# Kernel optimization log

Measured on AMD Instinct MI355X. Metric: run time of the kernel, lower is better.

The kernel has to match this reference:

```python
import jax, jax.numpy as jnp
import numpy as np

E = 200000   # edges (trade events)
N = 20000    # nodes
H = 128      # hidden_dim / memory_dim / time_dim
EF = 32      # edge_feat_dim
T = 14       # price_seq_dim
P = 4        # num_parties
S = 50       # num_states
LH = 32      # LSTM hidden


def setup_inputs() -> dict:
    key = jax.random.key(0)
    ks = jax.random.split(key, 32)
    rn = lambda k, shape, s=0.02: jax.random.normal(k, shape, dtype=jnp.float32) * s
    return {
        'src': jax.random.randint(ks[0], (E,), 0, N),
        'dst': jax.random.randint(ks[1], (E,), 0, N),
        't': jax.random.uniform(ks[2], (E,), dtype=jnp.float32) * 100.0,
        'msg': jax.random.normal(ks[3], (E, EF), dtype=jnp.float32),
        'price_seq': jax.random.normal(ks[4], (E, T), dtype=jnp.float32),
        'trade_t': jax.random.uniform(ks[5], (E,), dtype=jnp.float32),
        'x_static': jax.random.randint(ks[6], (N, 2), 0, P),
        # TGN memory state
        'memory': rn(ks[7], (N, H), 0.05),
        'last_update': jnp.zeros((N,), jnp.float32),
        # time encoder (cos(w*dt + b)), time_dim = H
        'time_w': rn(ks[8], (H,), 1.0),
        'time_b': rn(ks[9], (H,), 1.0),
        # GRU memory updater: input = [mem_src, mem_dst, raw_msg, t_enc] -> 3H+EF
        'gru_Wih': rn(ks[10], (3 * H, 3 * H + EF)),
        'gru_Whh': rn(ks[11], (3 * H, H)),
        'gru_bih': rn(ks[12], (3 * H,)),
        'gru_bhh': rn(ks[13], (3 * H,)),
        # static features
        'party_emb': rn(ks[14], (P, 16), 0.1),
        'state_emb': rn(ks[15], (S, 16), 0.1),
        'static_W': rn(ks[16], (H, 32)),
        'static_b': rn(ks[17], (H,)),
        # price LSTM (input_size=1, hidden=32); torch gate order i,f,g,o
        'lstm_Wih': rn(ks[18], (4 * LH, 1), 0.1),
        'lstm_Whh': rn(ks[19], (4 * LH, LH), 0.1),
        'lstm_bih': rn(ks[20], (4 * LH,), 0.1),
        'lstm_bhh': rn(ks[21], (4 * LH,), 0.1),
        'price_W': rn(ks[22], (H, LH)),
        'price_b': rn(ks[23], (H,)),
        # predictor MLP (dropout inactive at inference)
        'pred_W1': rn(ks[24], (64, 3 * H)),
        'pred_b1': rn(ks[25], (64,)),
        'pred_W2': rn(ks[26], (1, 64)),
        'pred_b2': rn(ks[27], (1,)),
    }


def reference(src, dst, t, msg, price_seq, trade_t, x_static,
              memory, last_update, time_w, time_b,
              gru_Wih, gru_Whh, gru_bih, gru_bhh,
              party_emb, state_emb, static_W, static_b,
              lstm_Wih, lstm_Whh, lstm_bih, lstm_bhh,
              price_W, price_b, pred_W1, pred_b1, pred_W2, pred_b2):
    n_nodes = memory.shape[0]

    # --- TGN memory update: scatter per-edge messages, GRU update, gather ---
    t_enc = lambda dt: jnp.cos(dt[:, None] * time_w[None, :] + time_b)  # [E,H]
    m_src, m_dst = memory[src], memory[dst]
    msg_to_dst = jnp.concatenate([m_src, m_dst, msg, t_enc(t - last_update[dst])], axis=1)
    msg_to_src = jnp.concatenate([m_dst, m_src, msg, t_enc(t - last_update[src])], axis=1)
    idx = jnp.concatenate([dst, src])                       # [2E]
    all_msgs = jnp.concatenate([msg_to_dst, msg_to_src], 0)  # [2E, 3H+EF]
    summed = jax.ops.segment_sum(all_msgs, idx, num_segments=n_nodes)
    count = jax.ops.segment_sum(jnp.ones((idx.shape[0],), jnp.float32), idx, num_segments=n_nodes)
    agg = summed / jnp.maximum(count, 1.0)[:, None]          # mean-aggregated message per node

    # GRUCell(agg, memory), torch semantics
    gi = agg @ gru_Wih.T + gru_bih
    gh = memory @ gru_Whh.T + gru_bhh
    i_r, i_z, i_n = jnp.split(gi, 3, axis=1)
    h_r, h_z, h_n = jnp.split(gh, 3, axis=1)
    r = jax.nn.sigmoid(i_r + h_r)
    z = jax.nn.sigmoid(i_z + h_z)
    n = jnp.tanh(i_n + r * h_n)
    h_new = (1.0 - z) * n + z * memory
    mem_new = jnp.where((count > 0)[:, None], h_new, memory)

    mem_src = mem_new[src]
    mem_dst = mem_new[dst]

    # --- static branch ---
    static_feat = jnp.concatenate([party_emb[x_static[src, 0]], state_emb[x_static[src, 1]]], axis=1)
    src_static = static_feat @ static_W.T + static_b

    # --- price LSTM branch ---
    e, lh = price_seq.shape[0], lstm_Whh.shape[1]

    def step(carry, x_t):
        h, c = carry
        g = x_t @ lstm_Wih.T + lstm_bih + h @ lstm_Whh.T + lstm_bhh
        gi_, gf_, gg_, go_ = jnp.split(g, 4, axis=1)
        c = jax.nn.sigmoid(gf_) * c + jax.nn.sigmoid(gi_) * jnp.tanh(gg_)
        h = jax.nn.sigmoid(go_) * jnp.tanh(c)
        return (h, c), None

    xs = price_seq.T[:, :, None]  # [T, E, 1]
    z0 = jnp.zeros((e, lh), price_seq.dtype)
    (h_n_last, _), _ = jax.lax.scan(step, (z0, z0), xs)
    price_emb = h_n_last @ price_W.T + price_b

    # --- fusion + predictor ---
    pol_ctx = mem_src + src_static
    comp_ctx = mem_dst + price_emb
    combined = jnp.concatenate([pol_ctx, comp_ctx, price_emb], axis=1)
    hid = jax.nn.relu(combined @ pred_W1.T + pred_b1)
    out = hid @ pred_W2.T + pred_b2
    return out.squeeze(-1)
```

## Files before the change

kernel.cpp:

```cpp
#include <hip/hip_runtime.h>

#define H 128
#define EF 32
#define TT 14
#define LH 32
#define KDIM 416
#define GOUT 512
#define KTOT 544
#define KP 288

typedef __attribute__((ext_vector_type(8))) short bf16x8;
typedef __attribute__((ext_vector_type(4))) float f32x4;

__device__ __forceinline__ float sigmoidf_(float x) {
  float e = __builtin_amdgcn_exp2f(x * -1.442695041f);
  return __builtin_amdgcn_rcpf(1.0f + e);
}
__device__ __forceinline__ float tanhfast_(float x) {
  float e = __builtin_amdgcn_exp2f(x * 2.885390082f);
  return 1.0f - 2.0f * __builtin_amdgcn_rcpf(e + 1.0f);
}
__device__ __forceinline__ ushort f2bf(float x) {
  uint u = __float_as_uint(x);
  u += 0x7fff + ((u >> 16) & 1);
  return (ushort)(u >> 16);
}

__global__ __launch_bounds__(256) void build_weights(
    const float* __restrict__ Wih, const float* __restrict__ Whh,
    ushort* __restrict__ WcatT) {
  int i = blockIdx.x * 256 + threadIdx.x;
  if (i >= GOUT * KTOT) return;
  int o = i / KTOT, k = i % KTOT;
  int j = o & 127;
  float v = 0.f;
  if (o < 256) {
    int row = (o < 128) ? j : (128 + j);
    v = (k < KDIM) ? Wih[row * KDIM + k] : Whh[row * H + (k - KDIM)];
  } else if (o < 384) {
    v = (k < KDIM) ? Wih[(256 + j) * KDIM + k] : 0.f;
  } else {
    v = (k < KDIM) ? 0.f : Whh[(256 + j) * H + (k - KDIM)];
  }
  WcatT[i] = f2bf(v);
}

__global__ __launch_bounds__(256) void prep_pred(
    const float* __restrict__ W1, const float* __restrict__ b1,
    const float* __restrict__ static_W, const float* __restrict__ static_b,
    const float* __restrict__ price_W, const float* __restrict__ price_b,
    const float* __restrict__ party_emb, const float* __restrict__ state_emb,
    ushort* __restrict__ Wcombb, float* __restrict__ tab_p, float* __restrict__ tab_s,
    float* __restrict__ bias2) {
  __shared__ float G1[64][32];
  int tid = threadIdx.x;
  for (int idx = tid; idx < 2048; idx += 256) {
    int o = idx >> 5, k = idx & 31;
    float g = 0.f, m = 0.f;
    for (int j = 0; j < 128; j++) {
      g = fmaf(W1[o * 384 + j], static_W[j * 32 + k], g);
      m = fmaf(W1[o * 384 + 128 + j] + W1[o * 384 + 256 + j], price_W[j * 32 + k], m);
    }
    G1[o][k] = g;
    Wcombb[o * KP + 256 + k] = f2bf(m);
  }
  for (int idx = tid; idx < 64 * 256; idx += 256) {
    int o = idx >> 8, j = idx & 255;
    Wcombb[o * KP + j] = f2bf(W1[o * 384 + j]);
  }
  __syncthreads();
  for (int idx = tid; idx < 4 * 64; idx += 256) {
    int p = idx >> 6, o = idx & 63;
    float s = 0.f;
    for (int k = 0; k < 16; k++) s = fmaf(G1[o][k], party_emb[p * 16 + k], s);
    tab_p[idx] = s;
  }
  for (int idx = tid; idx < 50 * 64; idx += 256) {
    int si = idx >> 6, o = idx & 63;
    float s = 0.f;
    for (int k = 0; k < 16; k++) s = fmaf(G1[o][16 + k], state_emb[si * 16 + k], s);
    tab_s[idx] = s;
  }
  if (tid < 64) {
    float s = b1[tid];
    for (int j = 0; j < 128; j++) {
      s = fmaf(W1[tid * 384 + j], static_b[j], s);
      s = fmaf(W1[tid * 384 + 128 + j] + W1[tid * 384 + 256 + j], price_b[j], s);
    }
    bias2[tid] = s;
  }
}

__global__ void count_kernel(const int* __restrict__ src, const int* __restrict__ dst,
                             int* cnt, int E) {
  int e = blockIdx.x * blockDim.x + threadIdx.x;
  if (e < E) {
    atomicAdd(&cnt[dst[e]], 1);
    atomicAdd(&cnt[src[e]], 1);
  }
}

__global__ __launch_bounds__(1024) void scan_kernel(const int* __restrict__ cnt,
                                                    int* __restrict__ offs,
                                                    int* __restrict__ cursor, int N) {
  __shared__ int part[1024];
  int tid = threadIdx.x;
  int chunk = (N + 1023) / 1024;
  int beg = tid * chunk;
  int end = min(beg + chunk, N);
  int s = 0;
  for (int i = beg; i < end; i++) s += cnt[i];
  part[tid] = s;
  __syncthreads();
  for (int d = 1; d < 1024; d <<= 1) {
    int v = (tid >= d) ? part[tid - d] : 0;
    __syncthreads();
    part[tid] += v;
    __syncthreads();
  }
  int run = (tid > 0) ? part[tid - 1] : 0;
  for (int i = beg; i < end; i++) {
    offs[i] = run;
    cursor[i] = run;
    run += cnt[i];
  }
  if (tid == 1023) offs[N] = part[1023];
}

__global__ void fill_kernel(const int* __restrict__ src, const int* __restrict__ dst,
                            int* cursor, int* __restrict__ other, int* __restrict__ eid, int E) {
  int e = blockIdx.x * blockDim.x + threadIdx.x;
  if (e >= E) return;
  int s = src[e], d = dst[e];
  int p1 = atomicAdd(&cursor[d], 1);
  other[p1] = s; eid[p1] = e;
  int p2 = atomicAdd(&cursor[s], 1);
  other[p2] = d; eid[p2] = e;
}

__global__ __launch_bounds__(512) void agg_kernel(
    const int* __restrict__ offs, const int* __restrict__ other, const int* __restrict__ eid,
    const float* __restrict__ mem, const float* __restrict__ msg,
    const float* __restrict__ t, const float* __restrict__ lu,
    const float* __restrict__ tw, const float* __restrict__ tb,
    const int* __restrict__ cnt, ushort* __restrict__ agg_b, int N) {
  __shared__ int ld_oth[256];
  __shared__ int ld_eid[256];
  __shared__ float red[16 * 292];
  int tid = threadIdx.x;
  int grp = tid >> 5;
  int l = tid & 31;
  int v = blockIdx.x;
  int beg = offs[v], end = offs[v + 1];
  int deg = end - beg;
  int ndeg = min(deg, 256);
  for (int i = tid; i < ndeg; i += 512) {
    ld_oth[i] = other[beg + i];
    ld_eid[i] = eid[beg + i];
  }
  __syncthreads();

  float lupd = lu[v];
  float4 w4 = *reinterpret_cast<const float4*>(tw + 4 * l);
  float4 b4 = *reinterpret_cast<const float4*>(tb + 4 * l);
  float a0q0 = 0.f, a0q1 = 0.f, a0q2 = 0.f, a0q3 = 0.f;
  float ac0 = 0.f, ac1 = 0.f, ac2 = 0.f, ac3 = 0.f;
  float amsg = 0.f;
  for (int p = grp; p < deg; p += 16) {
    int u, e;
    if (p < 256) { u = ld_oth[p]; e = ld_eid[p]; }
    else { u = other[beg + p]; e = eid[beg + p]; }
    float4 mrow = *reinterpret_cast<const float4*>(mem + (size_t)u * H + 4 * l);
    float te = t[e];
    amsg += msg[e * EF + l];
    float dt = te - lupd;
    a0q0 += mrow.x; a0q1 += mrow.y; a0q2 += mrow.z; a0q3 += mrow.w;
    ac0 += __cosf(fmaf(dt, w4.x, b4.x));
    ac1 += __cosf(fmaf(dt, w4.y, b4.y));
    ac2 += __cosf(fmaf(dt, w4.z, b4.z));
    ac3 += __cosf(fmaf(dt, w4.w, b4.w));
  }
  float* r = red + grp * 292;
  r[4 * l + 0] = a0q0; r[4 * l + 1] = a0q1; r[4 * l + 2] = a0q2; r[4 * l + 3] = a0q3;
  r[128 + 4 * l + 0] = ac0; r[128 + 4 * l + 1] = ac1;
  r[128 + 4 * l + 2] = ac2; r[128 + 4 * l + 3] = ac3;
  r[256 + l] = amsg;
  __syncthreads();

  int cv = cnt[v];
  float inv = 1.f / (float)max(cv, 1);
  ushort* arow = agg_b + (size_t)v * KTOT;
  if (tid < 288) {
    float s = 0.f;
#pragma unroll
    for (int g2 = 0; g2 < 16; g2++) s += red[g2 * 292 + tid];
    s *= inv;
    if (tid < 128) arow[tid] = f2bf(s);
    else if (tid < 256) arow[288 + (tid - 128)] = f2bf(s);
    else arow[256 + (tid - 256)] = f2bf(s);
  } else if (tid < 416) {
    int c = tid - 288;
    float mv = mem[(size_t)v * H + c];
    arow[128 + c] = f2bf((cv > 0) ? mv : 0.f);
    arow[416 + c] = f2bf(mv);
  }
}

__global__ __launch_bounds__(256) void gru_gemm_mfma(
    const ushort* __restrict__ aggb, const ushort* __restrict__ WcatT,
    const float* __restrict__ mem, const int* __restrict__ cnt,
    const float* __restrict__ bih, const float* __restrict__ bhh,
    ushort* __restrict__ mem_newb, int N) {
  __shared__ union {
    ushort a[32 * 552];
    float g[4][32][132];
  } sm;
  int tid = threadIdx.x;
  int lane = tid & 63;
  int w = tid >> 6;
  int n0 = blockIdx.x * 32;

#pragma unroll
  for (int i = 0; i < 8; i++) {
    int row = w * 8 + i;
    int gr = min(n0 + row, N - 1);
    const uint4* srcp = reinterpret_cast<const uint4*>(aggb + (size_t)gr * KTOT);
    uint4* dstp = reinterpret_cast<uint4*>(sm.a + row * 552);
    dstp[lane] = srcp[lane];
    if (lane < 4) dstp[64 + lane] = srcp[64 + lane];
  }
  __syncthreads();

  f32x4 acc[2][8] = {};
  int arow_b = (lane & 15);
  int koff = (lane >> 4) * 8;
  for (int ks = 0; ks < 17; ks++) {
    int k = ks * 32 + koff;
    bf16x8 afr0 = *reinterpret_cast<const bf16x8*>(sm.a + (arow_b) * 552 + k);
    bf16x8 afr1 = *reinterpret_cast<const bf16x8*>(sm.a + (16 + arow_b) * 552 + k);
#pragma unroll
    for (int nt = 0; nt < 8; nt++) {
      int o = w * 128 + nt * 16 + (lane & 15);
      bf16x8 bfr = *reinterpret_cast<const bf16x8*>(WcatT + (size_t)o * KTOT + k);
      acc[0][nt] = __builtin_amdgcn_mfma_f32_16x16x32_bf16(afr0, bfr, acc[0][nt], 0, 0, 0);
      acc[1][nt] = __builtin_amdgcn_mfma_f32_16x16x32_bf16(afr1, bfr, acc[1][nt], 0, 0, 0);
    }
  }
  __syncthreads();

#pragma unroll
  for (int mt = 0; mt < 2; mt++)
#pragma unroll
    for (int nt = 0; nt < 8; nt++)
#pragma unroll
      for (int r = 0; r < 4; r++)
        sm.g[w][mt * 16 + (lane >> 4) * 4 + r][nt * 16 + (lane & 15)] = acc[mt][nt][r];
  __syncthreads();

  int row = tid >> 3, j0 = (tid & 7) * 16;
  int n = n0 + row;
  if (n < N) {
    int cv = cnt[n];
#pragma unroll
    for (int jj = 0; jj < 16; jj++) {
      int j = j0 + jj;
      float m = mem[(size_t)n * H + j];
      float o;
      if (cv > 0) {
        float rp = sm.g[0][row][j] + bih[j] + bhh[j];
        float zp = sm.g[1][row][j] + bih[128 + j] + bhh[128 + j];
        float ip = sm.g[2][row][j] + bih[256 + j];
        float hp = sm.g[3][row][j] + bhh[256 + j];
        float r = sigmoidf_(rp), z = sigmoidf_(zp);
        float nn = tanhfast_(ip + r * hp);
        o = (1.f - z) * nn + z * m;
      } else {
        o = m;
      }
      mem_newb[(size_t)n * H + j] = f2bf(o);
    }
  }
}

__global__ __launch_bounds__(256) void lstm_mfma_kernel(
    const float* __restrict__ price_seq,
    const float* __restrict__ lWih, const float* __restrict__ lWhh,
    const float* __restrict__ lbih, const float* __restrict__ lbhh,
    ushort* __restrict__ houtb, int E) {
  __shared__ float ps[64][15];
  int tid = threadIdx.x;
  int lane = tid & 63;
  int el = lane & 15;
  int g = lane >> 4;
  int wv = tid >> 6;
  int row0 = blockIdx.x * 64;
  int el_local = wv * 16 + el;
  int e = row0 + el_local;
  bool valid = (e < E);

  for (int idx = tid; idx < 64 * TT; idx += 256) {
    int row = idx / TT, col = idx % TT;
    int ee = min(row0 + row, E - 1);
    ps[row][col] = price_seq[(size_t)ee * TT + col];
  }
  __syncthreads();

  union { uint u[4]; bf16x8 v; } afr[8];
#pragma unroll
  for (int b = 0; b < 8; b++) {
    const float* wr = lWhh + (16 * b + el) * LH + g * 8;
#pragma unroll
    for (int q = 0; q < 4; q++) {
      float lo = wr[2 * q], hi = wr[2 * q + 1];
      asm("v_cvt_pk_bf16_f32 %0, %1, %2" : "=v"(afr[b].u[q]) : "v"(lo), "v"(hi));
    }
  }
  uint afr2w[8];
#pragma unroll
  for (int b = 0; b < 8; b++) {
    float wvv = lWih[16 * b + el];
    float bv = lbih[16 * b + el] + lbhh[16 * b + el];
    uint pk;
    asm("v_cvt_pk_bf16_f32 %0, %1, %2" : "=v"(pk) : "v"(wvv), "v"(bv));
    afr2w[b] = (g == 0) ? pk : 0u;
  }

  int addr_i[4];
#pragma unroll
  for (int i = 0; i < 4; i++) addr_i[i] = (el + 16 * ((g & 1) * 2 + (i >> 1))) << 2;
  bool hi_sel = (g >> 1) != 0;

  float cst[8];
#pragma unroll
  for (int i = 0; i < 8; i++) cst[i] = 0.f;
  uint hpk[4] = {0u, 0u, 0u, 0u};
  const f32x4 zero4 = {0.f, 0.f, 0.f, 0.f};

#pragma unroll 1
  for (int t = 0; t < TT; t++) {
    union { uint u[4]; bf16x8 v; } bfr;
#pragma unroll
    for (int i = 0; i < 4; i++) {
      uint lo = (uint)__builtin_amdgcn_ds_bpermute(addr_i[i], (int)hpk[i & 1]);
      uint hi = (uint)__builtin_amdgcn_ds_bpermute(addr_i[i], (int)hpk[2 + (i & 1)]);
      bfr.u[i] = hi_sel ? hi : lo;
    }
    float x = ps[el_local][t];
    union { uint u[4]; bf16x8 v; } bfr2;
    uint xp;
    asm("v_cvt_pk_bf16_f32 %0, %1, %2" : "=v"(xp) : "v"(x), "v"(1.0f));
    bfr2.u[0] = (g == 0) ? xp : 0u;
    bfr2.u[1] = 0u; bfr2.u[2] = 0u; bfr2.u[3] = 0u;

    float hval[8];
    f32x4 acc0, acc1, acc2, acc3, acc4, acc5, acc6, acc7;
#define STEPACC(b, A) \
    { union { uint u[4]; bf16x8 v; } a2; a2.u[0] = afr2w[b]; a2.u[1] = 0u; a2.u[2] = 0u; a2.u[3] = 0u; \
      A = __builtin_amdgcn_mfma_f32_16x16x32_bf16(a2.v, bfr2.v, zero4, 0, 0, 0); \
      A = __builtin_amdgcn_mfma_f32_16x16x32_bf16(afr[b].v, bfr.v, A, 0, 0, 0); }
    STEPACC(0, acc0) STEPACC(1, acc1) STEPACC(2, acc2) STEPACC(3, acc3)
    STEPACC(4, acc4) STEPACC(5, acc5) STEPACC(6, acc6) STEPACC(7, acc7)
#undef STEPACC
#define NONLIN(b1, AI, AF, AG, AO) \
    { _Pragma("unroll") for (int r = 0; r < 4; r++) { \
        int mi = 4 * b1 + r; \
        float ig = sigmoidf_(AI[r]); \
        float fg = sigmoidf_(AF[r]); \
        float gg = tanhfast_(AG[r]); \
        float og = sigmoidf_(AO[r]); \
        float cv = fmaf(fg, cst[mi], ig * gg); \
        cst[mi] = cv; \
        hval[mi] = og * tanhfast_(cv); } }
    NONLIN(0, acc0, acc2, acc4, acc6)
    NONLIN(1, acc1, acc3, acc5, acc7)
#undef NONLIN
#pragma unroll
    for (int i = 0; i < 4; i++)
      asm("v_cvt_pk_bf16_f32 %0, %1, %2" : "=v"(hpk[i]) : "v"(hval[2 * i]), "v"(hval[2 * i + 1]));
  }

  if (valid) {
    uint2* rowp = reinterpret_cast<uint2*>(houtb + (size_t)e * LH);
    rowp[g] = make_uint2(hpk[0], hpk[1]);
    rowp[4 + g] = make_uint2(hpk[2], hpk[3]);
  }
}

__global__ __launch_bounds__(256) void pred_mfma(
    const int* __restrict__ src, const int* __restrict__ dst,
    const int* __restrict__ x_static,
    const ushort* __restrict__ mem_newb, const ushort* __restrict__ houtb,
    const ushort* __restrict__ Wcombb, const float* __restrict__ tab_p,
    const float* __restrict__ tab_s, const float* __restrict__ bias2,
    const float* __restrict__ W2, const float* __restrict__ b2,
    float* __restrict__ out, int E) {
  __shared__ ushort Asm[64 * 296];
  __shared__ int pidx[64], stix[64];
  __shared__ int sidx[64], didx[64];
  int tid = threadIdx.x;
  int row0 = blockIdx.x * 64;
  if (tid < 64) {
    int e = min(row0 + tid, E - 1);
    int s = src[e], d = dst[e];
    sidx[tid] = s; didx[tid] = d;
    pidx[tid] = x_static[s * 2]; stix[tid] = x_static[s * 2 + 1];
  }
  __syncthreads();
#pragma unroll
  for (int i = 0; i < 9; i++) {
    int idx = tid + i * 256;
    int row = idx / 36, c = idx % 36;
    int e = min(row0 + row, E - 1);
    uint4 v;
    if (c < 16) v = reinterpret_cast<const uint4*>(mem_newb + (size_t)sidx[row] * H)[c];
    else if (c < 32) v = reinterpret_cast<const uint4*>(mem_newb + (size_t)didx[row] * H)[c - 16];
    else v = reinterpret_cast<const uint4*>(houtb + (size_t)e * LH)[c - 32];
    *reinterpret_cast<uint4*>(Asm + row * 296 + c * 8) = v;
  }
  __syncthreads();

  int lane = tid & 63;
  int w = tid >> 6;
  f32x4 acc[4] = {};
  int arow = w * 16 + (lane & 15);
  int koff = (lane >> 4) * 8;
  for (int ks = 0; ks < 9; ks++) {
    int k = ks * 32 + koff;
    bf16x8 afr = *reinterpret_cast<const bf16x8*>(Asm + arow * 296 + k);
#pragma unroll
    for (int nt = 0; nt < 4; nt++) {
      int o = nt * 16 + (lane & 15);
      bf16x8 bfr = *reinterpret_cast<const bf16x8*>(Wcombb + (size_t)o * KP + k);
      acc[nt] = __builtin_amdgcn_mfma_f32_16x16x32_bf16(afr, bfr, acc[nt], 0, 0, 0);
    }
  }
  int ocol = lane & 15;
  float bb2 = b2[0];
#pragma unroll
  for (int r = 0; r < 4; r++) {
    int rl = w * 16 + (lane >> 4) * 4 + r;
    int p = pidx[rl], st = stix[rl];
    float s = 0.f;
#pragma unroll
    for (int nt = 0; nt < 4; nt++) {
      int o = nt * 16 + ocol;
      float hv = acc[nt][r] + bias2[o] + tab_p[p * 64 + o] + tab_s[st * 64 + o];
      s = fmaf(fmaxf(hv, 0.f), W2[o], s);
    }
#pragma unroll
    for (int d = 1; d < 16; d <<= 1) s += __shfl_xor(s, d);
    int e = row0 + rl;
    if (ocol == 0 && e < E) out[e] = s + bb2;
  }
}

extern "C" void kernel_launch(void* const* d_in, const int* in_sizes, int n_in,
                              void* d_out, int out_size, void* d_ws, size_t ws_size,
                              hipStream_t stream) {
  const int* src = (const int*)d_in[0];
  const int* dst = (const int*)d_in[1];
  const float* t = (const float*)d_in[2];
  const float* msg = (const float*)d_in[3];
  const float* price_seq = (const float*)d_in[4];
  const int* x_static = (const int*)d_in[6];
  const float* memory = (const float*)d_in[7];
  const float* last_update = (const float*)d_in[8];
  const float* time_w = (const float*)d_in[9];
  const float* time_b = (const float*)d_in[10];
  const float* gWih = (const float*)d_in[11];
  const float* gWhh = (const float*)d_in[12];
  const float* gbih = (const float*)d_in[13];
  const float* gbhh = (const float*)d_in[14];
  const float* party_emb = (const float*)d_in[15];
  const float* state_emb = (const float*)d_in[16];
  const float* static_W = (const float*)d_in[17];
  const float* static_b = (const float*)d_in[18];
  const float* lWih = (const float*)d_in[19];
  const float* lWhh = (const float*)d_in[20];
  const float* lbih = (const float*)d_in[21];
  const float* lbhh = (const float*)d_in[22];
  const float* price_W = (const float*)d_in[23];
  const float* price_b = (const float*)d_in[24];
  const float* W1 = (const float*)d_in[25];
  const float* b1 = (const float*)d_in[26];
  const float* W2 = (const float*)d_in[27];
  const float* b2 = (const float*)d_in[28];
  float* out = (float*)d_out;

  const int E = in_sizes[0];
  const int N = in_sizes[8];

  char* ws = (char*)d_ws;
  size_t off = 0;
  auto alloc = [&](size_t bytes) { size_t o = off; off += (bytes + 255) & ~(size_t)255; return o; };
  int* cnt       = (int*)(ws + alloc((size_t)N * 4));
  int* offs      = (int*)(ws + alloc((size_t)(N + 1) * 4));
  int* cursor    = (int*)(ws + alloc((size_t)N * 4));
  int* other     = (int*)(ws + alloc((size_t)2 * E * 4));
  int* eid       = (int*)(ws + alloc((size_t)2 * E * 4));
  ushort* WcatT  = (ushort*)(ws + alloc((size_t)GOUT * KTOT * 2));
  ushort* Wcombb = (ushort*)(ws + alloc((size_t)64 * KP * 2));
  float* tab_p   = (float*)(ws + alloc((size_t)4 * 64 * 4));
  float* tab_s   = (float*)(ws + alloc((size_t)50 * 64 * 4));
  float* bias2   = (float*)(ws + alloc((size_t)64 * 4));
  ushort* agg_b  = (ushort*)(ws + alloc((size_t)N * KTOT * 2));
  ushort* mem_newb = (ushort*)(ws + alloc((size_t)N * H * 2));
  ushort* houtb  = (ushort*)(ws + alloc((size_t)E * LH * 2));
  (void)ws_size;

  hipMemsetAsync(cnt, 0, (size_t)N * 4, stream);

  build_weights<<<(GOUT * KTOT + 255) / 256, 256, 0, stream>>>(gWih, gWhh, WcatT);
  prep_pred<<<1, 256, 0, stream>>>(W1, b1, static_W, static_b, price_W, price_b,
                                   party_emb, state_emb, Wcombb, tab_p, tab_s, bias2);
  count_kernel<<<(E + 255) / 256, 256, 0, stream>>>(src, dst, cnt, E);
  scan_kernel<<<1, 1024, 0, stream>>>(cnt, offs, cursor, N);
  fill_kernel<<<(E + 255) / 256, 256, 0, stream>>>(src, dst, cursor, other, eid, E);
  agg_kernel<<<N, 512, 0, stream>>>(offs, other, eid, memory, msg, t, last_update,
                                    time_w, time_b, cnt, agg_b, N);
  gru_gemm_mfma<<<(N + 31) / 32, 256, 0, stream>>>(agg_b, WcatT, memory, cnt,
                                                   gbih, gbhh, mem_newb, N);
  lstm_mfma_kernel<<<(E + 63) / 64, 256, 0, stream>>>(price_seq, lWih, lWhh, lbih, lbhh, houtb, E);
  pred_mfma<<<(E + 63) / 64, 256, 0, stream>>>(src, dst, x_static, mem_newb, houtb,
      Wcombb, tab_p, tab_s, bias2, W2, b2, out, E);
}
```

Measured before the change: 445.9 us.

## Fuse LSTM into aggregation launch and parallelize prep_pred across blocks

```diff
diff --git a/kernel.cpp b/kernel.cpp
--- a/kernel.cpp
+++ b/kernel.cpp
@@ -52,42 +52,48 @@
     const float* __restrict__ party_emb, const float* __restrict__ state_emb,
     ushort* __restrict__ Wcombb, float* __restrict__ tab_p, float* __restrict__ tab_s,
     float* __restrict__ bias2) {
-  __shared__ float G1[64][32];
+  __shared__ float G1s[4][32];
   int tid = threadIdx.x;
-  for (int idx = tid; idx < 2048; idx += 256) {
-    int o = idx >> 5, k = idx & 31;
+  int ob = blockIdx.x * 4;
+  if (tid < 128) {
+    int ol = tid >> 5, k = tid & 31;
+    int o = ob + ol;
     float g = 0.f, m = 0.f;
     for (int j = 0; j < 128; j++) {
       g = fmaf(W1[o * 384 + j], static_W[j * 32 + k], g);
       m = fmaf(W1[o * 384 + 128 + j] + W1[o * 384 + 256 + j], price_W[j * 32 + k], m);
     }
-    G1[o][k] = g;
+    G1s[ol][k] = g;
     Wcombb[o * KP + 256 + k] = f2bf(m);
   }
-  for (int idx = tid; idx < 64 * 256; idx += 256) {
-    int o = idx >> 8, j = idx & 255;
+  for (int idx = tid; idx < 1024; idx += 256) {
+    int ol = idx >> 8, j = idx & 255;
+    int o = ob + ol;
     Wcombb[o * KP + j] = f2bf(W1[o * 384 + j]);
   }
   __syncthreads();
-  for (int idx = tid; idx < 4 * 64; idx += 256) {
-    int p = idx >> 6, o = idx & 63;
-    float s = 0.f;
-    for (int k = 0; k < 16; k++) s = fmaf(G1[o][k], party_emb[p * 16 + k], s);
-    tab_p[idx] = s;
-  }
-  for (int idx = tid; idx < 50 * 64; idx += 256) {
-    int si = idx >> 6, o = idx & 63;
-    float s = 0.f;
-    for (int k = 0; k < 16; k++) s = fmaf(G1[o][16 + k], state_emb[si * 16 + k], s);
-    tab_s[idx] = s;
-  }
-  if (tid < 64) {
-    float s = b1[tid];
+  for (int idx = tid; idx < 216; idx += 256) {
+    if (idx < 16) {
+      int p = idx >> 2, ol = idx & 3;
+      float s = 0.f;
+      for (int k = 0; k < 16; k++) s = fmaf(G1s[ol][k], party_emb[p * 16 + k], s);
+      tab_p[p * 64 + ob + ol] = s;
+    } else {
+      int i2 = idx - 16;
+      int si = i2 >> 2, ol = i2 & 3;
+      float s = 0.f;
+      for (int k = 0; k < 16; k++) s = fmaf(G1s[ol][16 + k], state_emb[si * 16 + k], s);
+      tab_s[si * 64 + ob + ol] = s;
+    }
+  }
+  if (tid < 4) {
+    int o = ob + tid;
+    float s = b1[o];
     for (int j = 0; j < 128; j++) {
-      s = fmaf(W1[tid * 384 + j], static_b[j], s);
-      s = fmaf(W1[tid * 384 + 128 + j] + W1[tid * 384 + 256 + j], price_b[j], s);
-    }
-    bias2[tid] = s;
+      s = fmaf(W1[o * 384 + j], static_b[j], s);
+      s = fmaf(W1[o * 384 + 128 + j] + W1[o * 384 + 256 + j], price_b[j], s);
+    }
+    bias2[o] = s;
   }
 }
 
@@ -138,71 +144,175 @@
   other[p2] = d; eid[p2] = e;
 }
 
-__global__ __launch_bounds__(512) void agg_kernel(
+__global__ __launch_bounds__(512) void agg_lstm_kernel(
     const int* __restrict__ offs, const int* __restrict__ other, const int* __restrict__ eid,
     const float* __restrict__ mem, const float* __restrict__ msg,
     const float* __restrict__ t, const float* __restrict__ lu,
     const float* __restrict__ tw, const float* __restrict__ tb,
-    const int* __restrict__ cnt, ushort* __restrict__ agg_b, int N) {
-  __shared__ int ld_oth[256];
-  __shared__ int ld_eid[256];
-  __shared__ float red[16 * 292];
+    const int* __restrict__ cnt, ushort* __restrict__ agg_b, int N,
+    const float* __restrict__ price_seq,
+    const float* __restrict__ lWih, const float* __restrict__ lWhh,
+    const float* __restrict__ lbih, const float* __restrict__ lbhh,
+    ushort* __restrict__ houtb, int E, int nL) {
+  __shared__ union {
+    struct { int ld_oth[256]; int ld_eid[256]; float red[16 * 292]; } a;
+    float ps[128][15];
+  } sm;
   int tid = threadIdx.x;
-  int grp = tid >> 5;
-  int l = tid & 31;
-  int v = blockIdx.x;
-  int beg = offs[v], end = offs[v + 1];
-  int deg = end - beg;
-  int ndeg = min(deg, 256);
-  for (int i = tid; i < ndeg; i += 512) {
-    ld_oth[i] = other[beg + i];
-    ld_eid[i] = eid[beg + i];
-  }
-  __syncthreads();
-
-  float lupd = lu[v];
-  float4 w4 = *reinterpret_cast<const float4*>(tw + 4 * l);
-  float4 b4 = *reinterpret_cast<const float4*>(tb + 4 * l);
-  float a0q0 = 0.f, a0q1 = 0.f, a0q2 = 0.f, a0q3 = 0.f;
-  float ac0 = 0.f, ac1 = 0.f, ac2 = 0.f, ac3 = 0.f;
-  float amsg = 0.f;
-  for (int p = grp; p < deg; p += 16) {
-    int u, e;
-    if (p < 256) { u = ld_oth[p]; e = ld_eid[p]; }
-    else { u = other[beg + p]; e = eid[beg + p]; }
-    float4 mrow = *reinterpret_cast<const float4*>(mem + (size_t)u * H + 4 * l);
-    float te = t[e];
-    amsg += msg[e * EF + l];
-    float dt = te - lupd;
-    a0q0 += mrow.x; a0q1 += mrow.y; a0q2 += mrow.z; a0q3 += mrow.w;
-    ac0 += __cosf(fmaf(dt, w4.x, b4.x));
-    ac1 += __cosf(fmaf(dt, w4.y, b4.y));
-    ac2 += __cosf(fmaf(dt, w4.z, b4.z));
-    ac3 += __cosf(fmaf(dt, w4.w, b4.w));
-  }
-  float* r = red + grp * 292;
-  r[4 * l + 0] = a0q0; r[4 * l + 1] = a0q1; r[4 * l + 2] = a0q2; r[4 * l + 3] = a0q3;
-  r[128 + 4 * l + 0] = ac0; r[128 + 4 * l + 1] = ac1;
-  r[128 + 4 * l + 2] = ac2; r[128 + 4 * l + 3] = ac3;
-  r[256 + l] = amsg;
-  __syncthreads();
-
-  int cv = cnt[v];
-  float inv = 1.f / (float)max(cv, 1);
-  ushort* arow = agg_b + (size_t)v * KTOT;
-  if (tid < 288) {
-    float s = 0.f;
-#pragma unroll
-    for (int g2 = 0; g2 < 16; g2++) s += red[g2 * 292 + tid];
-    s *= inv;
-    if (tid < 128) arow[tid] = f2bf(s);
-    else if (tid < 256) arow[288 + (tid - 128)] = f2bf(s);
-    else arow[256 + (tid - 256)] = f2bf(s);
-  } else if (tid < 416) {
-    int c = tid - 288;
-    float mv = mem[(size_t)v * H + c];
-    arow[128 + c] = f2bf((cv > 0) ? mv : 0.f);
-    arow[416 + c] = f2bf(mv);
+
+  if ((int)blockIdx.x < nL) {
+    int lane = tid & 63;
+    int el = lane & 15;
+    int g = lane >> 4;
+    int wv = tid >> 6;
+    int row0 = blockIdx.x * 128;
+    int el_local = wv * 16 + el;
+    int e = row0 + el_local;
+    bool valid = (e < E);
+
+    for (int idx = tid; idx < 128 * TT; idx += 512) {
+      int row = idx / TT, col = idx % TT;
+      int ee = min(row0 + row, E - 1);
+      sm.ps[row][col] = price_seq[(size_t)ee * TT + col];
+    }
+    __syncthreads();
+
+    union { uint u[4]; bf16x8 v; } afr[8];
+#pragma unroll
+    for (int b = 0; b < 8; b++) {
+      const float* wr = lWhh + (16 * b + el) * LH + g * 8;
+#pragma unroll
+      for (int q = 0; q < 4; q++) {
+        float lo = wr[2 * q], hi = wr[2 * q + 1];
+        asm("v_cvt_pk_bf16_f32 %0, %1, %2" : "=v"(afr[b].u[q]) : "v"(lo), "v"(hi));
+      }
+    }
+    uint afr2w[8];
+#pragma unroll
+    for (int b = 0; b < 8; b++) {
+      float wvv = lWih[16 * b + el];
+      float bv = lbih[16 * b + el] + lbhh[16 * b + el];
+      uint pk;
+      asm("v_cvt_pk_bf16_f32 %0, %1, %2" : "=v"(pk) : "v"(wvv), "v"(bv));
+      afr2w[b] = (g == 0) ? pk : 0u;
+    }
+
+    int addr_i[4];
+#pragma unroll
+    for (int i = 0; i < 4; i++) addr_i[i] = (el + 16 * ((g & 1) * 2 + (i >> 1))) << 2;
+    bool hi_sel = (g >> 1) != 0;
+
+    float cst[8];
+#pragma unroll
+    for (int i = 0; i < 8; i++) cst[i] = 0.f;
+    uint hpk[4] = {0u, 0u, 0u, 0u};
+    const f32x4 zero4 = {0.f, 0.f, 0.f, 0.f};
+
+#pragma unroll 1
+    for (int tt = 0; tt < TT; tt++) {
+      union { uint u[4]; bf16x8 v; } bfr;
+#pragma unroll
+      for (int i = 0; i < 4; i++) {
+        uint lo = (uint)__builtin_amdgcn_ds_bpermute(addr_i[i], (int)hpk[i & 1]);
+        uint hi = (uint)__builtin_amdgcn_ds_bpermute(addr_i[i], (int)hpk[2 + (i & 1)]);
+        bfr.u[i] = hi_sel ? hi : lo;
+      }
+      float x = sm.ps[el_local][tt];
+      union { uint u[4]; bf16x8 v; } bfr2;
+      uint xp;
+      asm("v_cvt_pk_bf16_f32 %0, %1, %2" : "=v"(xp) : "v"(x), "v"(1.0f));
+      bfr2.u[0] = (g == 0) ? xp : 0u;
+      bfr2.u[1] = 0u; bfr2.u[2] = 0u; bfr2.u[3] = 0u;
+
+      float hval[8];
+      f32x4 acc0, acc1, acc2, acc3, acc4, acc5, acc6, acc7;
+#define STEPACC(b, A) \
+      { union { uint u[4]; bf16x8 v; } a2; a2.u[0] = afr2w[b]; a2.u[1] = 0u; a2.u[2] = 0u; a2.u[3] = 0u; \
+        A = __builtin_amdgcn_mfma_f32_16x16x32_bf16(a2.v, bfr2.v, zero4, 0, 0, 0); \
+        A = __builtin_amdgcn_mfma_f32_16x16x32_bf16(afr[b].v, bfr.v, A, 0, 0, 0); }
+      STEPACC(0, acc0) STEPACC(1, acc1) STEPACC(2, acc2) STEPACC(3, acc3)
+      STEPACC(4, acc4) STEPACC(5, acc5) STEPACC(6, acc6) STEPACC(7, acc7)
+#undef STEPACC
+#define NONLIN(b1, AI, AF, AG, AO) \
+      { _Pragma("unroll") for (int r = 0; r < 4; r++) { \
+          int mi = 4 * b1 + r; \
+          float ig = sigmoidf_(AI[r]); \
+          float fg = sigmoidf_(AF[r]); \
+          float gg = tanhfast_(AG[r]); \
+          float og = sigmoidf_(AO[r]); \
+          float cv = fmaf(fg, cst[mi], ig * gg); \
+          cst[mi] = cv; \
+          hval[mi] = og * tanhfast_(cv); } }
+      NONLIN(0, acc0, acc2, acc4, acc6)
+      NONLIN(1, acc1, acc3, acc5, acc7)
+#undef NONLIN
+#pragma unroll
+      for (int i = 0; i < 4; i++)
+        asm("v_cvt_pk_bf16_f32 %0, %1, %2" : "=v"(hpk[i]) : "v"(hval[2 * i]), "v"(hval[2 * i + 1]));
+    }
+
+    if (valid) {
+      uint2* rowp = reinterpret_cast<uint2*>(houtb + (size_t)e * LH);
+      rowp[g] = make_uint2(hpk[0], hpk[1]);
+      rowp[4 + g] = make_uint2(hpk[2], hpk[3]);
+    }
+  } else {
+    int grp = tid >> 5;
+    int l = tid & 31;
+    int v = blockIdx.x - nL;
+    int beg = offs[v], end = offs[v + 1];
+    int deg = end - beg;
+    int ndeg = min(deg, 256);
+    for (int i = tid; i < ndeg; i += 512) {
+      sm.a.ld_oth[i] = other[beg + i];
+      sm.a.ld_eid[i] = eid[beg + i];
+    }
+    __syncthreads();
+
+    float lupd = lu[v];
+    float4 w4 = *reinterpret_cast<const float4*>(tw + 4 * l);
+    float4 b4 = *reinterpret_cast<const float4*>(tb + 4 * l);
+    float a0q0 = 0.f, a0q1 = 0.f, a0q2 = 0.f, a0q3 = 0.f;
+    float ac0 = 0.f, ac1 = 0.f, ac2 = 0.f, ac3 = 0.f;
+    float amsg = 0.f;
+    for (int p = grp; p < deg; p += 16) {
+      int u, e;
+      if (p < 256) { u = sm.a.ld_oth[p]; e = sm.a.ld_eid[p]; }
+      else { u = other[beg + p]; e = eid[beg + p]; }
+      float4 mrow = *reinterpret_cast<const float4*>(mem + (size_t)u * H + 4 * l);
+      float te = t[e];
+      amsg += msg[e * EF + l];
+      float dt = te - lupd;
+      a0q0 += mrow.x; a0q1 += mrow.y; a0q2 += mrow.z; a0q3 += mrow.w;
+      ac0 += __cosf(fmaf(dt, w4.x, b4.x));
+      ac1 += __cosf(fmaf(dt, w4.y, b4.y));
+      ac2 += __cosf(fmaf(dt, w4.z, b4.z));
+      ac3 += __cosf(fmaf(dt, w4.w, b4.w));
+    }
+    float* r = sm.a.red + grp * 292;
+    r[4 * l + 0] = a0q0; r[4 * l + 1] = a0q1; r[4 * l + 2] = a0q2; r[4 * l + 3] = a0q3;
+    r[128 + 4 * l + 0] = ac0; r[128 + 4 * l + 1] = ac1;
+    r[128 + 4 * l + 2] = ac2; r[128 + 4 * l + 3] = ac3;
+    r[256 + l] = amsg;
+    __syncthreads();
+
+    int cv = cnt[v];
+    float inv = 1.f / (float)max(cv, 1);
+    ushort* arow = agg_b + (size_t)v * KTOT;
+    if (tid < 288) {
+      float s = 0.f;
+#pragma unroll
+      for (int g2 = 0; g2 < 16; g2++) s += sm.a.red[g2 * 292 + tid];
+      s *= inv;
+      if (tid < 128) arow[tid] = f2bf(s);
+      else if (tid < 256) arow[288 + (tid - 128)] = f2bf(s);
+      else arow[256 + (tid - 256)] = f2bf(s);
+    } else if (tid < 416) {
+      int c = tid - 288;
+      float mv = mem[(size_t)v * H + c];
+      arow[128 + c] = f2bf((cv > 0) ? mv : 0.f);
+      arow[416 + c] = f2bf(mv);
+    }
   }
 }
 
@@ -279,110 +389,6 @@
       }
       mem_newb[(size_t)n * H + j] = f2bf(o);
     }
-  }
-}
-
-__global__ __launch_bounds__(256) void lstm_mfma_kernel(
-    const float* __restrict__ price_seq,
-    const float* __restrict__ lWih, const float* __restrict__ lWhh,
-    const float* __restrict__ lbih, const float* __restrict__ lbhh,
-    ushort* __restrict__ houtb, int E) {
-  __shared__ float ps[64][15];
-  int tid = threadIdx.x;
-  int lane = tid & 63;
-  int el = lane & 15;
-  int g = lane >> 4;
-  int wv = tid >> 6;
-  int row0 = blockIdx.x * 64;
-  int el_local = wv * 16 + el;
-  int e = row0 + el_local;
-  bool valid = (e < E);
-
-  for (int idx = tid; idx < 64 * TT; idx += 256) {
-    int row = idx / TT, col = idx % TT;
-    int ee = min(row0 + row, E - 1);
-    ps[row][col] = price_seq[(size_t)ee * TT + col];
-  }
-  __syncthreads();
-
-  union { uint u[4]; bf16x8 v; } afr[8];
-#pragma unroll
-  for (int b = 0; b < 8; b++) {
-    const float* wr = lWhh + (16 * b + el) * LH + g * 8;
-#pragma unroll
-    for (int q = 0; q < 4; q++) {
-      float lo = wr[2 * q], hi = wr[2 * q + 1];
-      asm("v_cvt_pk_bf16_f32 %0, %1, %2" : "=v"(afr[b].u[q]) : "v"(lo), "v"(hi));
-    }
-  }
-  uint afr2w[8];
-#pragma unroll
-  for (int b = 0; b < 8; b++) {
-    float wvv = lWih[16 * b + el];
-    float bv = lbih[16 * b + el] + lbhh[16 * b + el];
-    uint pk;
-    asm("v_cvt_pk_bf16_f32 %0, %1, %2" : "=v"(pk) : "v"(wvv), "v"(bv));
-    afr2w[b] = (g == 0) ? pk : 0u;
-  }
-
-  int addr_i[4];
-#pragma unroll
-  for (int i = 0; i < 4; i++) addr_i[i] = (el + 16 * ((g & 1) * 2 + (i >> 1))) << 2;
-  bool hi_sel = (g >> 1) != 0;
-
-  float cst[8];
-#pragma unroll
-  for (int i = 0; i < 8; i++) cst[i] = 0.f;
-  uint hpk[4] = {0u, 0u, 0u, 0u};
-  const f32x4 zero4 = {0.f, 0.f, 0.f, 0.f};
-
-#pragma unroll 1
-  for (int t = 0; t < TT; t++) {
-    union { uint u[4]; bf16x8 v; } bfr;
-#pragma unroll
-    for (int i = 0; i < 4; i++) {
-      uint lo = (uint)__builtin_amdgcn_ds_bpermute(addr_i[i], (int)hpk[i & 1]);
-      uint hi = (uint)__builtin_amdgcn_ds_bpermute(addr_i[i], (int)hpk[2 + (i & 1)]);
-      bfr.u[i] = hi_sel ? hi : lo;
-    }
-    float x = ps[el_local][t];
-    union { uint u[4]; bf16x8 v; } bfr2;
-    uint xp;
-    asm("v_cvt_pk_bf16_f32 %0, %1, %2" : "=v"(xp) : "v"(x), "v"(1.0f));
-    bfr2.u[0] = (g == 0) ? xp : 0u;
-    bfr2.u[1] = 0u; bfr2.u[2] = 0u; bfr2.u[3] = 0u;
-
-    float hval[8];
-    f32x4 acc0, acc1, acc2, acc3, acc4, acc5, acc6, acc7;
-#define STEPACC(b, A) \
-    { union { uint u[4]; bf16x8 v; } a2; a2.u[0] = afr2w[b]; a2.u[1] = 0u; a2.u[2] = 0u; a2.u[3] = 0u; \
-      A = __builtin_amdgcn_mfma_f32_16x16x32_bf16(a2.v, bfr2.v, zero4, 0, 0, 0); \
-      A = __builtin_amdgcn_mfma_f32_16x16x32_bf16(afr[b].v, bfr.v, A, 0, 0, 0); }
-    STEPACC(0, acc0) STEPACC(1, acc1) STEPACC(2, acc2) STEPACC(3, acc3)
-    STEPACC(4, acc4) STEPACC(5, acc5) STEPACC(6, acc6) STEPACC(7, acc7)
-#undef STEPACC
-#define NONLIN(b1, AI, AF, AG, AO) \
-    { _Pragma("unroll") for (int r = 0; r < 4; r++) { \
-        int mi = 4 * b1 + r; \
-        float ig = sigmoidf_(AI[r]); \
-        float fg = sigmoidf_(AF[r]); \
-        float gg = tanhfast_(AG[r]); \
-        float og = sigmoidf_(AO[r]); \
-        float cv = fmaf(fg, cst[mi], ig * gg); \
-        cst[mi] = cv; \
-        hval[mi] = og * tanhfast_(cv); } }
-    NONLIN(0, acc0, acc2, acc4, acc6)
-    NONLIN(1, acc1, acc3, acc5, acc7)
-#undef NONLIN
-#pragma unroll
-    for (int i = 0; i < 4; i++)
-      asm("v_cvt_pk_bf16_f32 %0, %1, %2" : "=v"(hpk[i]) : "v"(hval[2 * i]), "v"(hval[2 * i + 1]));
-  }
-
-  if (valid) {
-    uint2* rowp = reinterpret_cast<uint2*>(houtb + (size_t)e * LH);
-    rowp[g] = make_uint2(hpk[0], hpk[1]);
-    rowp[4 + g] = make_uint2(hpk[2], hpk[3]);
   }
 }
 
@@ -511,16 +517,17 @@
   hipMemsetAsync(cnt, 0, (size_t)N * 4, stream);
 
   build_weights<<<(GOUT * KTOT + 255) / 256, 256, 0, stream>>>(gWih, gWhh, WcatT);
-  prep_pred<<<1, 256, 0, stream>>>(W1, b1, static_W, static_b, price_W, price_b,
-                                   party_emb, state_emb, Wcombb, tab_p, tab_s, bias2);
+  prep_pred<<<16, 256, 0, stream>>>(W1, b1, static_W, static_b, price_W, price_b,
+                                    party_emb, state_emb, Wcombb, tab_p, tab_s, bias2);
   count_kernel<<<(E + 255) / 256, 256, 0, stream>>>(src, dst, cnt, E);
   scan_kernel<<<1, 1024, 0, stream>>>(cnt, offs, cursor, N);
   fill_kernel<<<(E + 255) / 256, 256, 0, stream>>>(src, dst, cursor, other, eid, E);
-  agg_kernel<<<N, 512, 0, stream>>>(offs, other, eid, memory, msg, t, last_update,
-                                    time_w, time_b, cnt, agg_b, N);
+  int nL = (E + 127) / 128;
+  agg_lstm_kernel<<<nL + N, 512, 0, stream>>>(offs, other, eid, memory, msg, t, last_update,
+                                              time_w, time_b, cnt, agg_b, N,
+                                              price_seq, lWih, lWhh, lbih, lbhh, houtb, E, nL);
   gru_gemm_mfma<<<(N + 31) / 32, 256, 0, stream>>>(agg_b, WcatT, memory, cnt,
                                                    gbih, gbhh, mem_newb, N);
-  lstm_mfma_kernel<<<(E + 63) / 64, 256, 0, stream>>>(price_seq, lWih, lWhh, lbih, lbhh, houtb, E);
   pred_mfma<<<(E + 63) / 64, 256, 0, stream>>>(src, dst, x_static, mem_newb, houtb,
       Wcombb, tab_p, tab_s, bias2, W2, b2, out, E);
 }
```

Measured after the change: 423.9 us. 4.9% less time.
